# Optimization experiments

Hardware: AMD Instinct MI355X
Metric: run time of the kernel (lower is better)

The kernel has to match this reference:

```python
import jax, jax.numpy as jnp
import numpy as np

NUM_WIRES = 14
N_LAYERS = 2
BATCH = 256
DIM = 2 ** NUM_WIRES


def setup_inputs() -> dict:
    key = jax.random.key(0)
    k1, k2, k3 = jax.random.split(key, 3)
    s = jax.random.normal(k1, (BATCH, DIM), dtype=jnp.float32)
    # StatePrep requires normalized amplitudes
    s = s / jnp.linalg.norm(s, axis=1, keepdims=True)
    params = jax.random.normal(k2, (N_LAYERS, NUM_WIRES, 3), dtype=jnp.float32)
    head_w = jax.random.normal(k3, (1, NUM_WIRES), dtype=jnp.float32) / np.sqrt(NUM_WIRES)
    head_b = jnp.zeros((1,), dtype=jnp.float32)
    return {"state_batch": s, "params": params, "head_w": head_w, "head_b": head_b}


def _ry(t):
    c = jnp.cos(t / 2).astype(jnp.complex64)
    s = jnp.sin(t / 2).astype(jnp.complex64)
    return jnp.stack([jnp.stack([c, -s]), jnp.stack([s, c])])


def _rz(t):
    tc = t.astype(jnp.complex64)
    e_m = jnp.exp(-0.5j * tc)
    e_p = jnp.exp(0.5j * tc)
    z = jnp.zeros((), jnp.complex64)
    return jnp.stack([jnp.stack([e_m, z]), jnp.stack([z, e_p])])


def _rx(t):
    c = jnp.cos(t / 2).astype(jnp.complex64)
    s = (-1j) * jnp.sin(t / 2).astype(jnp.complex64)
    return jnp.stack([jnp.stack([c, s]), jnp.stack([s, c])])


def _apply_1q(psi, U, wire):
    # psi: (B, 2, 2, ..., 2); contract 2x2 gate on axis wire+1 across the batch
    out = jnp.tensordot(U, psi, axes=([1], [wire + 1]))
    return jnp.moveaxis(out, 0, wire + 1)


def _apply_cnot(psi, control, target):
    # flip target axis where control bit == 1
    shape = [1] * psi.ndim
    shape[control + 1] = 2
    mask = (jnp.arange(2) == 1).reshape(shape)
    return jnp.where(mask, jnp.flip(psi, axis=target + 1), psi)


def _circuit(state_c, params):
    psi = state_c.reshape((BATCH,) + (2,) * NUM_WIRES)
    for layer in range(N_LAYERS):
        for w in range(NUM_WIRES):
            psi = _apply_1q(psi, _ry(params[layer, w, 0]), w)
            psi = _apply_1q(psi, _rz(params[layer, w, 1]), w)
            psi = _apply_cnot(psi, w, (w + 1) % NUM_WIRES)
            psi = _apply_1q(psi, _rx(params[layer, w, 2]), w)
    probs = (psi.real ** 2 + psi.imag ** 2).reshape(BATCH, DIM)
    # <Z_w> = sum over basis states of prob * (+1/-1 depending on bit of wire w)
    basis = jnp.arange(DIM)
    shifts = NUM_WIRES - 1 - jnp.arange(NUM_WIRES)  # wire 0 is the MSB axis
    signs = 1.0 - 2.0 * ((basis[None, :] >> shifts[:, None]) & 1).astype(jnp.float32)
    return probs @ signs.T  # (B, NUM_WIRES)


def reference(state_batch, params, head_w, head_b):
    feats = _circuit(state_batch.astype(jnp.complex64), params)  # (B, NUM_WIRES)
    return feats @ head_w[0] + head_b[0]  # (B,)
```

## Files before the change

kernel.cpp:

```cpp
#include <hip/hip_runtime.h>
#include <math.h>

typedef float v2f __attribute__((ext_vector_type(2)));

constexpr int NW = 14;
constexpr int DIM = 1 << NW;
constexpr int BATCH = 256;
constexpr int NT = 512;

__device__ __forceinline__ int swz(int i) { return i ^ ((i >> 5) & 31); }

template<int JW, int JT>
__device__ __forceinline__ void gate_u(v2f (&pr)[16], v2f (&pi)[16],
                                       float cy, float sy, float c1, float s1,
                                       float cx, float sx)
{
    constexpr int BW = 1 << JW, BT = 1 << JT;
    #pragma unroll
    for (int m = 0; m < 4; ++m) {
        int l00 = 0, mm = m;
        #pragma unroll
        for (int j = 0; j < 4; ++j)
            if (j != JW && j != JT) { l00 |= (mm & 1) << j; mm >>= 1; }
        const int iA = l00, iB = l00 | BW, iC = l00 | BT, iD = l00 | BW | BT;

        v2f a00r = pr[iA], a00i = pi[iA];
        v2f a10r = pr[iB], a10i = pi[iB];
        v2f a01r = pr[iC], a01i = pi[iC];
        v2f a11r = pr[iD], a11i = pi[iD];

        v2f v0r = cy*a00r - sy*a10r, v0i = cy*a00i - sy*a10i;
        v2f v1r = sy*a00r + cy*a10r, v1i = sy*a00i + cy*a10i;
        v2f u0r = cy*a01r - sy*a11r, u0i = cy*a01i - sy*a11i;
        v2f u1r = sy*a01r + cy*a11r, u1i = sy*a01i + cy*a11i;

        v2f b00r = c1*v0r + s1*v0i, b00i = c1*v0i - s1*v0r;
        v2f b10r = c1*v1r - s1*v1i, b10i = c1*v1i + s1*v1r;
        v2f b01r = c1*u0r + s1*u0i, b01i = c1*u0i - s1*u0r;
        v2f b11r = c1*u1r - s1*u1i, b11i = c1*u1i + s1*u1r;

        v2f o00r = cx*b00r + sx*b11i, o00i = cx*b00i - sx*b11r;
        v2f o10r = sx*b00i + cx*b11r, o10i = cx*b11i - sx*b00r;
        v2f o01r = cx*b01r + sx*b10i, o01i = cx*b01i - sx*b10r;
        v2f o11r = sx*b01i + cx*b10r, o11i = cx*b10i - sx*b01r;

        pr[iA] = o00r; pi[iA] = o00i;
        pr[iB] = o10r; pi[iB] = o10i;
        pr[iC] = o01r; pi[iC] = o01i;
        pr[iD] = o11r; pi[iD] = o11i;
    }
}

__device__ __forceinline__ void gate_c(v2f (&pr)[16], v2f (&pi)[16],
                                       float cy, float sy, float c1, float s1,
                                       float cx, float sx)
{
    #pragma unroll
    for (int m = 0; m < 8; ++m) {
        const int iA = m << 1, iB = iA | 1;
        v2f Ar = pr[iA], Ai = pi[iA];
        v2f Br = pr[iB], Bi = pi[iB];

        v2f Vr = cy*Ar - sy*Br, Vi = cy*Ai - sy*Bi;
        v2f Wr = sy*Ar + cy*Br, Wi = sy*Ai + cy*Bi;

        v2f P0r = c1*Vr + s1*Vi, P0i = c1*Vi - s1*Vr;
        v2f P1r = c1*Wr - s1*Wi, P1i = c1*Wi + s1*Wr;

        v2f sP1r = {P1r.y, P1r.x};
        v2f sP1i = {P1i.y, P1i.x};

        pr[iA] = cx*P0r + sx*sP1i;
        pi[iA] = cx*P0i - sx*sP1r;
        pr[iB] = sx*P0i + cx*sP1r;
        pi[iB] = cx*sP1i - sx*P0r;
    }
}

template<int P0, int P1, int P2, int P3, int P4>
__device__ __forceinline__ int base_of(int t)
{
    int base = 0, j = 0;
    #pragma unroll
    for (int p = 0; p < NW; ++p) {
        if (p != P0 && p != P1 && p != P2 && p != P3 && p != P4) {
            base |= ((t >> j) & 1) << p;
            ++j;
        }
    }
    return base;
}

template<int P0, int P1, int P2, int P3, int P4>
__device__ __forceinline__ int off_of(int l)
{
    return ((l & 1) << P0) | (((l >> 1) & 1) << P1) | (((l >> 2) & 1) << P2) |
           (((l >> 3) & 1) << P3) | (((l >> 4) & 1) << P4);
}

template<int P0, int P1, int P2, int P3, int P4>
__device__ __forceinline__ void lds_load_pk(const float* re, const float* im,
                                            v2f (&pr)[16], v2f (&pi)[16], int base)
{
    #pragma unroll
    for (int k = 0; k < 16; ++k) {
        const int s0 = swz(base | off_of<P0, P1, P2, P3, P4>(k));
        const int s1_ = swz(base | off_of<P0, P1, P2, P3, P4>(k | 16));
        pr[k] = v2f{re[s0], re[s1_]};
        pi[k] = v2f{im[s0], im[s1_]};
    }
}

template<int P0, int P1, int P2, int P3, int P4>
__device__ __forceinline__ void lds_store_pk(float* re, float* im,
                                             const v2f (&pr)[16], const v2f (&pi)[16], int base)
{
    #pragma unroll
    for (int k = 0; k < 16; ++k) {
        const int s0 = swz(base | off_of<P0, P1, P2, P3, P4>(k));
        const int s1_ = swz(base | off_of<P0, P1, P2, P3, P4>(k | 16));
        re[s0] = pr[k].x; re[s1_] = pr[k].y;
        im[s0] = pi[k].x; im[s1_] = pi[k].y;
    }
}

__global__ __launch_bounds__(NT, 1) void qsim(const float* __restrict__ state,
                                              const float* __restrict__ params,
                                              const float* __restrict__ head_w,
                                              const float* __restrict__ head_b,
                                              float* __restrict__ out)
{
    __shared__ float re[DIM];
    __shared__ float im[DIM];
    __shared__ float2 csv[NW * 3 * 2];
    __shared__ float partial[NT / 64];

    const int t = threadIdx.x;
    const int b = blockIdx.x;

    v2f pr[16], pi[16];

    const float* __restrict__ sp = state + (size_t)b * DIM;
    #pragma unroll
    for (int k = 0; k < 16; ++k) {
        pr[k] = v2f{sp[t | (k << 10)], sp[t | (k << 10) | 512]};
        pi[k] = v2f{0.0f, 0.0f};
    }

    if (t < NW * 3 * 2) {
        float sv, cv;
        sincosf(params[t] * 0.5f, &sv, &cv);
        csv[t] = make_float2(cv, sv);
    }
    __syncthreads();

#define GATEU(JW, JT, G) do {                                           \
        float2 vy = csv[(G) * 3 + 0];                                   \
        float2 vz = csv[(G) * 3 + 1];                                   \
        float2 vx = csv[(G) * 3 + 2];                                   \
        gate_u<JW, JT>(pr, pi, vy.x, vy.y, vz.x, vz.y, vx.x, vx.y);     \
    } while (0)
#define GATEC(G) do {                                                   \
        float2 vy = csv[(G) * 3 + 0];                                   \
        float2 vz = csv[(G) * 3 + 1];                                   \
        float2 vx = csv[(G) * 3 + 2];                                   \
        gate_c(pr, pi, vy.x, vy.y, vz.x, vz.y, vx.x, vx.y);             \
    } while (0)


    GATEU(3, 2, 0); GATEU(2, 1, 1); GATEU(1, 0, 2); GATEC(3);
    lds_store_pk<10, 11, 12, 13, 9>(re, im, pr, pi, base_of<10, 11, 12, 13, 9>(t));
    __syncthreads();

    {
        const int base = base_of<6, 7, 8, 9, 5>(t);
        lds_load_pk<6, 7, 8, 9, 5>(re, im, pr, pi, base);
        GATEU(3, 2, 4); GATEU(2, 1, 5); GATEU(1, 0, 6); GATEC(7);
        lds_store_pk<6, 7, 8, 9, 5>(re, im, pr, pi, base);
    }
    __syncthreads();

    {
        const int base = base_of<2, 3, 4, 5, 1>(t);
        lds_load_pk<2, 3, 4, 5, 1>(re, im, pr, pi, base);
        GATEU(3, 2, 8); GATEU(2, 1, 9); GATEU(1, 0, 10); GATEC(11);
        lds_store_pk<2, 3, 4, 5, 1>(re, im, pr, pi, base);
    }
    __syncthreads();

    {
        const int base = base_of<12, 13, 0, 1, 11>(t);
        lds_load_pk<12, 13, 0, 1, 11>(re, im, pr, pi, base);
        GATEU(3, 2, 12); GATEU(2, 1, 13); GATEU(1, 0, 14); GATEC(15);
        lds_store_pk<12, 13, 0, 1, 11>(re, im, pr, pi, base);
    }
    __syncthreads();

    {
        const int base = base_of<8, 9, 10, 11, 7>(t);
        lds_load_pk<8, 9, 10, 11, 7>(re, im, pr, pi, base);
        GATEU(3, 2, 16); GATEU(2, 1, 17); GATEU(1, 0, 18); GATEC(19);
        lds_store_pk<8, 9, 10, 11, 7>(re, im, pr, pi, base);
    }
    __syncthreads();

    {
        const int base = base_of<4, 5, 6, 7, 3>(t);
        lds_load_pk<4, 5, 6, 7, 3>(re, im, pr, pi, base);
        GATEU(3, 2, 20); GATEU(2, 1, 21); GATEU(1, 0, 22); GATEC(23);
        lds_store_pk<4, 5, 6, 7, 3>(re, im, pr, pi, base);
    }
    __syncthreads();

    {
        const int base = base_of<0, 1, 2, 3, 13>(t);
        lds_load_pk<0, 1, 2, 3, 13>(re, im, pr, pi, base);
        GATEU(3, 2, 24); GATEU(2, 1, 25); GATEU(1, 0, 26); GATEC(27);
    }

    float hw[NW];
    #pragma unroll
    for (int w = 0; w < NW; ++w) hw[w] = head_w[w];

    float gbase = 0.0f;
    #pragma unroll
    for (int j = 0; j < 9; ++j) {
        float h = hw[9 - j];
        gbase += ((t >> j) & 1) ? -h : h;
    }

    v2f acc2 = {0.0f, 0.0f};
    #pragma unroll
    for (int k = 0; k < 16; ++k) {
        float gk = gbase;
        gk += (k & 1) ? -hw[13] : hw[13];
        gk += (k & 2) ? -hw[12] : hw[12];
        gk += (k & 4) ? -hw[11] : hw[11];
        gk += (k & 8) ? -hw[10] : hw[10];
        v2f g = {gk + hw[0], gk - hw[0]};
        acc2 += (pr[k] * pr[k] + pi[k] * pi[k]) * g;
    }
    float acc = acc2.x + acc2.y;

    #pragma unroll
    for (int off = 32; off > 0; off >>= 1) acc += __shfl_down(acc, off);
    if ((t & 63) == 0) partial[t >> 6] = acc;
    __syncthreads();
    if (t == 0) {
        float tot = 0.0f;
        #pragma unroll
        for (int k = 0; k < NT / 64; ++k) tot += partial[k];
        out[b] = tot + head_b[0];
    }
#undef GATEU
#undef GATEC
}

extern "C" void kernel_launch(void* const* d_in, const int* in_sizes, int n_in,
                              void* d_out, int out_size, void* d_ws, size_t ws_size,
                              hipStream_t stream) {
    const float* state  = (const float*)d_in[0];
    const float* params = (const float*)d_in[1];
    const float* head_w = (const float*)d_in[2];
    const float* head_b = (const float*)d_in[3];
    float* outp = (float*)d_out;
    qsim<<<BATCH, NT, 0, stream>>>(state, params, head_w, head_b, outp);
}
```

Measured before the change: 36.31 us.

## Use cross-lane permlane swaps to cut LDS exchange rounds

Reorganizes the qubit-to-register/lane mapping so that some gate groups are handled by exchanging qubits between lane halves with v_permlane32/16_swap instead of shared-memory round trips. This reduces the number of LDS store/load phases and block barriers, and adds a new gate kernel that works on a lane-resident qubit plus a new swizzle. The cost is extra permlane instructions with s_nop padding and a more intricate index mapping that must be exactly right.

```diff
diff --git a/kernel.cpp b/kernel.cpp
--- a/kernel.cpp
+++ b/kernel.cpp
@@ -8,7 +8,16 @@
 constexpr int BATCH = 256;
 constexpr int NT = 512;
 
-__device__ __forceinline__ int swz(int i) { return i ^ ((i >> 5) & 31); }
+__device__ __host__ constexpr int swzc(int i) {
+    return i ^ ((i >> 5) & 31) ^ (((i >> 10) & 15) << 1);
+}
+
+template<int Q0,int Q1,int Q2,int Q3,int Q4,int Q5,int Q6,int Q7,int Q8>
+__device__ __forceinline__ int scat9(int t) {
+    return ((t & 1) << Q0) | (((t >> 1) & 1) << Q1) | (((t >> 2) & 1) << Q2) |
+           (((t >> 3) & 1) << Q3) | (((t >> 4) & 1) << Q4) | (((t >> 5) & 1) << Q5) |
+           (((t >> 6) & 1) << Q6) | (((t >> 7) & 1) << Q7) | (((t >> 8) & 1) << Q8);
+}
 
 template<int JW, int JT>
 __device__ __forceinline__ void gate_u(v2f (&pr)[16], v2f (&pi)[16],
@@ -51,76 +60,101 @@
     }
 }
 
-__device__ __forceinline__ void gate_c(v2f (&pr)[16], v2f (&pi)[16],
+template<int JT>
+__device__ __forceinline__ void gate_w(v2f (&pr)[16], v2f (&pi)[16],
                                        float cy, float sy, float c1, float s1,
                                        float cx, float sx)
 {
+    constexpr int BT = 1 << JT;
+    const v2f K1 = {cy, sy};
+    const v2f K2 = {-sy, cy};
+    const v2f Zs = {s1, -s1};
     #pragma unroll
     for (int m = 0; m < 8; ++m) {
-        const int iA = m << 1, iB = iA | 1;
+        int l00 = 0, mm = m;
+        #pragma unroll
+        for (int j = 0; j < 4; ++j)
+            if (j != JT) { l00 |= (mm & 1) << j; mm >>= 1; }
+        const int iA = l00, iB = l00 | BT;
         v2f Ar = pr[iA], Ai = pi[iA];
         v2f Br = pr[iB], Bi = pi[iB];
 
-        v2f Vr = cy*Ar - sy*Br, Vi = cy*Ai - sy*Bi;
-        v2f Wr = sy*Ar + cy*Br, Wi = sy*Ai + cy*Bi;
-
-        v2f P0r = c1*Vr + s1*Vi, P0i = c1*Vi - s1*Vr;
-        v2f P1r = c1*Wr - s1*Wi, P1i = c1*Wi + s1*Wr;
-
-        v2f sP1r = {P1r.y, P1r.x};
-        v2f sP1i = {P1i.y, P1i.x};
-
-        pr[iA] = cx*P0r + sx*sP1i;
-        pi[iA] = cx*P0i - sx*sP1r;
-        pr[iB] = sx*P0i + cx*sP1r;
-        pi[iB] = cx*sP1i - sx*P0r;
-    }
-}
-
-template<int P0, int P1, int P2, int P3, int P4>
-__device__ __forceinline__ int base_of(int t)
-{
-    int base = 0, j = 0;
-    #pragma unroll
-    for (int p = 0; p < NW; ++p) {
-        if (p != P0 && p != P1 && p != P2 && p != P3 && p != P4) {
-            base |= ((t >> j) & 1) << p;
-            ++j;
-        }
-    }
-    return base;
-}
-
-template<int P0, int P1, int P2, int P3, int P4>
-__device__ __forceinline__ int off_of(int l)
-{
-    return ((l & 1) << P0) | (((l >> 1) & 1) << P1) | (((l >> 2) & 1) << P2) |
-           (((l >> 3) & 1) << P3) | (((l >> 4) & 1) << P4);
-}
-
-template<int P0, int P1, int P2, int P3, int P4>
-__device__ __forceinline__ void lds_load_pk(const float* re, const float* im,
-                                            v2f (&pr)[16], v2f (&pi)[16], int base)
-{
-    #pragma unroll
-    for (int k = 0; k < 16; ++k) {
-        const int s0 = swz(base | off_of<P0, P1, P2, P3, P4>(k));
-        const int s1_ = swz(base | off_of<P0, P1, P2, P3, P4>(k | 16));
-        pr[k] = v2f{re[s0], re[s1_]};
-        pi[k] = v2f{im[s0], im[s1_]};
-    }
-}
-
-template<int P0, int P1, int P2, int P3, int P4>
-__device__ __forceinline__ void lds_store_pk(float* re, float* im,
-                                             const v2f (&pr)[16], const v2f (&pi)[16], int base)
-{
-    #pragma unroll
-    for (int k = 0; k < 16; ++k) {
-        const int s0 = swz(base | off_of<P0, P1, P2, P3, P4>(k));
-        const int s1_ = swz(base | off_of<P0, P1, P2, P3, P4>(k | 16));
-        re[s0] = pr[k].x; re[s1_] = pr[k].y;
-        im[s0] = pi[k].x; im[s1_] = pi[k].y;
+        v2f vAr = K1*Ar.xx + K2*Ar.yy;
+        v2f vAi = K1*Ai.xx + K2*Ai.yy;
+        v2f vBr = K1*Br.xx + K2*Br.yy;
+        v2f vBi = K1*Bi.xx + K2*Bi.yy;
+        v2f bAr = c1*vAr + Zs*vAi;
+        v2f bAi = c1*vAi - Zs*vAr;
+        v2f bBr = c1*vBr + Zs*vBi;
+        v2f bBi = c1*vBi - Zs*vBr;
+        v2f t1  = {bAr.x, bBr.y};
+        v2f t1p = {bBr.x, bAr.y};
+        v2f t2  = {bAi.x, bBi.y};
+        v2f t2p = {bBi.x, bAi.y};
+        pr[iA] = cx*t1  + sx*t2.yx;
+        pi[iA] = cx*t2  - sx*t1.yx;
+        pr[iB] = cx*t1p + sx*t2p.yx;
+        pi[iB] = cx*t2p - sx*t1p.yx;
+    }
+}
+
+template<int J>
+__device__ __forceinline__ void swap_l5(v2f (&pr)[16], v2f (&pi)[16]) {
+    #pragma unroll
+    for (int m = 0; m < 8; ++m) {
+        int l0 = 0, mm = m;
+        #pragma unroll
+        for (int j = 0; j < 4; ++j)
+            if (j != J) { l0 |= (mm & 1) << j; mm >>= 1; }
+        const int l1 = l0 | (1 << J);
+        { float a=pr[l0].x, c=pr[l1].x; asm("s_nop 1\n\tv_permlane32_swap_b32 %0, %1":"+v"(a),"+v"(c)); pr[l0].x=a; pr[l1].x=c; }
+        { float a=pr[l0].y, c=pr[l1].y; asm("s_nop 1\n\tv_permlane32_swap_b32 %0, %1":"+v"(a),"+v"(c)); pr[l0].y=a; pr[l1].y=c; }
+        { float a=pi[l0].x, c=pi[l1].x; asm("s_nop 1\n\tv_permlane32_swap_b32 %0, %1":"+v"(a),"+v"(c)); pi[l0].x=a; pi[l1].x=c; }
+        { float a=pi[l0].y, c=pi[l1].y; asm("s_nop 1\n\tv_permlane32_swap_b32 %0, %1":"+v"(a),"+v"(c)); pi[l0].y=a; pi[l1].y=c; }
+    }
+}
+
+template<int J>
+__device__ __forceinline__ void swap_l4(v2f (&pr)[16], v2f (&pi)[16]) {
+    #pragma unroll
+    for (int m = 0; m < 8; ++m) {
+        int l0 = 0, mm = m;
+        #pragma unroll
+        for (int j = 0; j < 4; ++j)
+            if (j != J) { l0 |= (mm & 1) << j; mm >>= 1; }
+        const int l1 = l0 | (1 << J);
+        { float a=pr[l0].x, c=pr[l1].x; asm("s_nop 1\n\tv_permlane16_swap_b32 %0, %1":"+v"(a),"+v"(c)); pr[l0].x=a; pr[l1].x=c; }
+        { float a=pr[l0].y, c=pr[l1].y; asm("s_nop 1\n\tv_permlane16_swap_b32 %0, %1":"+v"(a),"+v"(c)); pr[l0].y=a; pr[l1].y=c; }
+        { float a=pi[l0].x, c=pi[l1].x; asm("s_nop 1\n\tv_permlane16_swap_b32 %0, %1":"+v"(a),"+v"(c)); pi[l0].x=a; pi[l1].x=c; }
+        { float a=pi[l0].y, c=pi[l1].y; asm("s_nop 1\n\tv_permlane16_swap_b32 %0, %1":"+v"(a),"+v"(c)); pi[l0].y=a; pi[l1].y=c; }
+    }
+}
+
+template<int A0,int A1,int A2,int A3,int PP>
+__device__ __forceinline__ void lds_load(const float* re, const float* im,
+                                         v2f (&pr)[16], v2f (&pi)[16], int sb) {
+    #pragma unroll
+    for (int l = 0; l < 16; ++l) {
+        const int off = ((l & 1) << A0) | (((l >> 1) & 1) << A1) |
+                        (((l >> 2) & 1) << A2) | (((l >> 3) & 1) << A3);
+        const int s0 = sb ^ swzc(off);
+        const int s1 = sb ^ swzc(off | (1 << PP));
+        pr[l] = v2f{re[s0], re[s1]};
+        pi[l] = v2f{im[s0], im[s1]};
+    }
+}
+
+template<int A0,int A1,int A2,int A3,int PP>
+__device__ __forceinline__ void lds_store(float* re, float* im,
+                                          const v2f (&pr)[16], const v2f (&pi)[16], int sb) {
+    #pragma unroll
+    for (int l = 0; l < 16; ++l) {
+        const int off = ((l & 1) << A0) | (((l >> 1) & 1) << A1) |
+                        (((l >> 2) & 1) << A2) | (((l >> 3) & 1) << A3);
+        const int s0 = sb ^ swzc(off);
+        const int s1 = sb ^ swzc(off | (1 << PP));
+        re[s0] = pr[l].x; re[s1] = pr[l].y;
+        im[s0] = pi[l].x; im[s1] = pi[l].y;
     }
 }
 
@@ -141,10 +175,13 @@
     v2f pr[16], pi[16];
 
     const float* __restrict__ sp = state + (size_t)b * DIM;
-    #pragma unroll
-    for (int k = 0; k < 16; ++k) {
-        pr[k] = v2f{sp[t | (k << 10)], sp[t | (k << 10) | 512]};
-        pi[k] = v2f{0.0f, 0.0f};
+    const int tb1 = scat9<0,1,2,3,7,8,4,5,6>(t);
+    #pragma unroll
+    for (int l = 0; l < 16; ++l) {
+        const int off = ((l & 1) << 9) | (((l >> 1) & 1) << 10) |
+                        (((l >> 2) & 1) << 11) | (((l >> 3) & 1) << 12);
+        pr[l] = v2f{sp[tb1 | off], sp[tb1 | off | (1 << 13)]};
+        pi[l] = v2f{0.0f, 0.0f};
     }
 
     if (t < NW * 3 * 2) {
@@ -154,91 +191,93 @@
     }
     __syncthreads();
 
-#define GATEU(JW, JT, G) do {                                           \
-        float2 vy = csv[(G) * 3 + 0];                                   \
-        float2 vz = csv[(G) * 3 + 1];                                   \
-        float2 vx = csv[(G) * 3 + 2];                                   \
+#define GU(JW, JT, G) do {                                              \
+        float2 vy = csv[(G)*3+0], vz = csv[(G)*3+1], vx = csv[(G)*3+2]; \
         gate_u<JW, JT>(pr, pi, vy.x, vy.y, vz.x, vz.y, vx.x, vx.y);     \
     } while (0)
-#define GATEC(G) do {                                                   \
-        float2 vy = csv[(G) * 3 + 0];                                   \
-        float2 vz = csv[(G) * 3 + 1];                                   \
-        float2 vx = csv[(G) * 3 + 2];                                   \
-        gate_c(pr, pi, vy.x, vy.y, vz.x, vz.y, vx.x, vx.y);             \
+#define GW(JT, G) do {                                                  \
+        float2 vy = csv[(G)*3+0], vz = csv[(G)*3+1], vx = csv[(G)*3+2]; \
+        gate_w<JT>(pr, pi, vy.x, vy.y, vz.x, vz.y, vx.x, vx.y);         \
     } while (0)
 
-
-    GATEU(3, 2, 0); GATEU(2, 1, 1); GATEU(1, 0, 2); GATEC(3);
-    lds_store_pk<10, 11, 12, 13, 9>(re, im, pr, pi, base_of<10, 11, 12, 13, 9>(t));
-    __syncthreads();
-
-    {
-        const int base = base_of<6, 7, 8, 9, 5>(t);
-        lds_load_pk<6, 7, 8, 9, 5>(re, im, pr, pi, base);
-        GATEU(3, 2, 4); GATEU(2, 1, 5); GATEU(1, 0, 6); GATEC(7);
-        lds_store_pk<6, 7, 8, 9, 5>(re, im, pr, pi, base);
-    }
-    __syncthreads();
-
-    {
-        const int base = base_of<2, 3, 4, 5, 1>(t);
-        lds_load_pk<2, 3, 4, 5, 1>(re, im, pr, pi, base);
-        GATEU(3, 2, 8); GATEU(2, 1, 9); GATEU(1, 0, 10); GATEC(11);
-        lds_store_pk<2, 3, 4, 5, 1>(re, im, pr, pi, base);
-    }
-    __syncthreads();
-
-    {
-        const int base = base_of<12, 13, 0, 1, 11>(t);
-        lds_load_pk<12, 13, 0, 1, 11>(re, im, pr, pi, base);
-        GATEU(3, 2, 12); GATEU(2, 1, 13); GATEU(1, 0, 14); GATEC(15);
-        lds_store_pk<12, 13, 0, 1, 11>(re, im, pr, pi, base);
-    }
-    __syncthreads();
-
-    {
-        const int base = base_of<8, 9, 10, 11, 7>(t);
-        lds_load_pk<8, 9, 10, 11, 7>(re, im, pr, pi, base);
-        GATEU(3, 2, 16); GATEU(2, 1, 17); GATEU(1, 0, 18); GATEC(19);
-        lds_store_pk<8, 9, 10, 11, 7>(re, im, pr, pi, base);
-    }
-    __syncthreads();
-
-    {
-        const int base = base_of<4, 5, 6, 7, 3>(t);
-        lds_load_pk<4, 5, 6, 7, 3>(re, im, pr, pi, base);
-        GATEU(3, 2, 20); GATEU(2, 1, 21); GATEU(1, 0, 22); GATEC(23);
-        lds_store_pk<4, 5, 6, 7, 3>(re, im, pr, pi, base);
-    }
-    __syncthreads();
-
-    {
-        const int base = base_of<0, 1, 2, 3, 13>(t);
-        lds_load_pk<0, 1, 2, 3, 13>(re, im, pr, pi, base);
-        GATEU(3, 2, 24); GATEU(2, 1, 25); GATEU(1, 0, 26); GATEC(27);
-    }
+    GW(3, 0);
+    GU(3, 2, 1);
+    GU(2, 1, 2);
+    GU(1, 0, 3);
+    swap_l5<3>(pr, pi);
+    GU(0, 3, 4);
+    swap_l4<0>(pr, pi);
+    GU(3, 0, 5);
+    lds_store<7,10,11,8,13>(re, im, pr, pi, swzc(scat9<0,1,2,3,9,12,4,5,6>(t)));
+    __syncthreads();
+
+    lds_load<3,4,5,6,7>(re, im, pr, pi, swzc(scat9<0,8,9,11,1,2,10,12,13>(t)));
+    GW(3, 6);
+    GU(3, 2, 7);
+    GU(2, 1, 8);
+    GU(1, 0, 9);
+    swap_l5<3>(pr, pi);
+    GU(0, 3, 10);
+    swap_l4<2>(pr, pi);
+    GU(3, 2, 11);
+    lds_store<3,4,1,2,7>(re, im, pr, pi, swzc(scat9<0,8,9,11,5,6,10,12,13>(t)));
+    __syncthreads();
+
+    lds_load<0,13,12,11,1>(re, im, pr, pi, swzc(scat9<2,5,6,3,9,10,4,7,8>(t)));
+    GW(0, 12);
+    GU(0, 1, 13);
+    GU(1, 2, 14);
+    GU(2, 3, 15);
+    swap_l5<1>(pr, pi);
+    GU(3, 1, 16);
+    swap_l4<0>(pr, pi);
+    GU(1, 0, 17);
+    lds_store<9,10,12,11,1>(re, im, pr, pi, swzc(scat9<2,5,6,3,0,13,4,7,8>(t)));
+    __syncthreads();
+
+    lds_load<8,7,6,5,9>(re, im, pr, pi, swzc(scat9<0,1,2,13,3,4,10,11,12>(t)));
+    GW(0, 18);
+    GU(0, 1, 19);
+    GU(1, 2, 20);
+    GU(2, 3, 21);
+    swap_l5<0>(pr, pi);
+    GU(3, 0, 22);
+    swap_l4<1>(pr, pi);
+    GU(0, 1, 23);
+    lds_store<4,3,6,5,9>(re, im, pr, pi, swzc(scat9<0,1,2,13,7,8,10,11,12>(t)));
+    __syncthreads();
+
+    lds_load<2,1,0,13,3>(re, im, pr, pi, swzc(scat9<4,5,6,7,8,9,10,11,12>(t)));
+    GW(0, 24);
+    GU(0, 1, 25);
+    GU(1, 2, 26);
+    GU(2, 3, 27);
 
     float hw[NW];
     #pragma unroll
     for (int w = 0; w < NW; ++w) hw[w] = head_w[w];
 
     float gbase = 0.0f;
-    #pragma unroll
-    for (int j = 0; j < 9; ++j) {
-        float h = hw[9 - j];
-        gbase += ((t >> j) & 1) ? -h : h;
-    }
+    gbase += (t & 1)   ? -hw[9] : hw[9];
+    gbase += (t & 2)   ? -hw[8] : hw[8];
+    gbase += (t & 4)   ? -hw[7] : hw[7];
+    gbase += (t & 8)   ? -hw[6] : hw[6];
+    gbase += (t & 16)  ? -hw[5] : hw[5];
+    gbase += (t & 32)  ? -hw[4] : hw[4];
+    gbase += (t & 64)  ? -hw[3] : hw[3];
+    gbase += (t & 128) ? -hw[2] : hw[2];
+    gbase += (t & 256) ? -hw[1] : hw[1];
 
     v2f acc2 = {0.0f, 0.0f};
     #pragma unroll
-    for (int k = 0; k < 16; ++k) {
-        float gk = gbase;
-        gk += (k & 1) ? -hw[13] : hw[13];
-        gk += (k & 2) ? -hw[12] : hw[12];
-        gk += (k & 4) ? -hw[11] : hw[11];
-        gk += (k & 8) ? -hw[10] : hw[10];
-        v2f g = {gk + hw[0], gk - hw[0]};
-        acc2 += (pr[k] * pr[k] + pi[k] * pi[k]) * g;
+    for (int l = 0; l < 16; ++l) {
+        float g = gbase;
+        g += (l & 1) ? -hw[11] : hw[11];
+        g += (l & 2) ? -hw[12] : hw[12];
+        g += (l & 4) ? -hw[13] : hw[13];
+        g += (l & 8) ? -hw[0]  : hw[0];
+        v2f gv = {g + hw[10], g - hw[10]};
+        acc2 += (pr[l]*pr[l] + pi[l]*pi[l]) * gv;
     }
     float acc = acc2.x + acc2.y;
 
@@ -252,8 +291,8 @@
         for (int k = 0; k < NT / 64; ++k) tot += partial[k];
         out[b] = tot + head_b[0];
     }
-#undef GATEU
-#undef GATEC
+#undef GU
+#undef GW
 }
 
 extern "C" void kernel_launch(void* const* d_in, const int* in_sizes, int n_in,
```

After: 37.56 us. 1.03x slower.
